# Kernel optimization log

Measured on AMD Instinct MI355X. Metric: run time of the kernel, lower is better.

## Reference

```python
import jax, jax.numpy as jnp
import numpy as np

N_NODES = 50000
N_EDGES = 800000
NFEAT, NHID, NCLASS = 256, 64, 2


def _deg_norm(idx, n_nodes, dtype):
    deg = jax.ops.segment_sum(jnp.ones(idx.shape[0], dtype=dtype), idx, num_segments=n_nodes)
    return jax.lax.rsqrt(jnp.maximum(deg, 1.0))


def gcn_layer(x, W, b, src, dst, n_nodes):
    # DGL GraphConv, norm='both': h = D_in^{-1/2} * Agg( D_out^{-1/2} * x ) W + b
    # weight applied before aggregation (in_feats >= out_feats path); math-equivalent.
    norm_src = _deg_norm(src, n_nodes, x.dtype)  # out-degree norm of source nodes
    norm_dst = _deg_norm(dst, n_nodes, x.dtype)  # in-degree norm of dest nodes
    h = (x * norm_src[:, None]) @ W              # [N, out]
    agg = jax.ops.segment_sum(h[src], dst, num_segments=n_nodes)  # gather + scatter-add
    return agg * norm_dst[:, None] + b


def setup_inputs() -> dict:
    key = jax.random.key(0)
    k1, k2, k3, k4, k5, k6, k7 = jax.random.split(key, 7)
    x = jax.random.normal(k1, (N_NODES, NFEAT), dtype=jnp.float32)
    src = jax.random.randint(k2, (N_EDGES,), 0, N_NODES, dtype=jnp.int64)
    dst = jax.random.randint(k3, (N_EDGES,), 0, N_NODES, dtype=jnp.int64)
    # Glorot-style init like DGL GraphConv
    W1 = jax.random.normal(k4, (NFEAT, NHID), dtype=jnp.float32) * (2.0 / (NFEAT + NHID)) ** 0.5
    b1 = jnp.zeros((NHID,), dtype=jnp.float32)
    W2 = jax.random.normal(k5, (NHID, NCLASS), dtype=jnp.float32) * (2.0 / (NHID + NCLASS)) ** 0.5
    b2 = jnp.zeros((NCLASS,), dtype=jnp.float32)
    return {"x": x, "src": src, "dst": dst, "W1": W1, "b1": b1, "W2": W2, "b2": b2}


def reference(x, src, dst, W1, b1, W2, b2):
    h = jax.nn.relu(gcn_layer(x, W1, b1, src, dst, N_NODES))
    # dropout=False -> p=0, no-op
    logits = gcn_layer(h, W2, b2, src, dst, N_NODES)
    return jax.nn.log_softmax(logits, axis=1)
```

## Files before the change

kernel.cpp:

```cpp
#include <hip/hip_runtime.h>
#include <math.h>

#define N_NODES 50000
#define N_EDGES 800000
#define NFEAT 256
#define NHID 64
#define NCLASS 2

#define DB 64
#define NDB 782
#define BCAP 1536
#define EPB 2048
#define NB_EDGE ((N_EDGES + EPB - 1) / EPB)

#define OFF_CURD 0
#define OFF_CURS 800
#define OFF_RBD  1600
#define OFF_NDST 101600
#define OFF_NSRC 151600
#define OFF_W1T  201600
#define OFF_DPK  209792
#define OFF_SV6  1410944
#define OFF_CSR  1711232
#define OFF_HB   2912384
#define OFF_H2   4512384

typedef __attribute__((ext_vector_type(8))) short bf16x8;
typedef __attribute__((ext_vector_type(8))) short short8;
typedef __attribute__((ext_vector_type(4))) float f32x4;

static __device__ __forceinline__ unsigned short f2bf(float f) {
    union { float f; unsigned int u; } v; v.f = f;
    return (unsigned short)((v.u + 0x8000u) >> 16);
}
static __device__ __forceinline__ unsigned int pk2bf(float f0, float f1) {
    union { float f; unsigned int u; } a, b; a.f = f0; b.f = f1;
    return __builtin_amdgcn_perm(b.u + 0x8000u, a.u + 0x8000u, 0x07060302u);
}
static __device__ __forceinline__ float bflo(unsigned int u) {
    union { unsigned int x; float f; } v; v.x = u << 16; return v.f;
}
static __device__ __forceinline__ float bfhi(unsigned int u) {
    union { unsigned int x; float f; } v; v.x = u & 0xffff0000u; return v.f;
}

#define INIT_N (1600 + NFEAT * NHID)
__global__ __launch_bounds__(256) void init_kernel(const float* __restrict__ W1,
                                                   int* __restrict__ cursors,
                                                   unsigned short* __restrict__ w1t) {
    int g = blockIdx.x * 256 + threadIdx.x;
    if (g < 1600) {
        cursors[g] = 0;
    } else if (g < INIT_N) {
        int idx = g - 1600;
        int k = idx >> 6, n = idx & 63;
        w1t[n * NFEAT + k] = f2bf(W1[idx]);
    }
}

union SgShared {
    struct { int hd[NDB], bd[NDB], cd[NDB], hs[NDB], bs[NDB], cs[NDB]; } b;
    struct { unsigned short As[64][136]; unsigned short Bs[64][136]; } g;
};
__global__ __launch_bounds__(256) void sg_kernel(const int* __restrict__ src,
                                                 const int* __restrict__ dst,
                                                 const float* __restrict__ x,
                                                 const unsigned short* __restrict__ w1t,
                                                 int* __restrict__ cur_d,
                                                 int* __restrict__ cur_s,
                                                 int* __restrict__ dpk,
                                                 unsigned char* __restrict__ sv6,
                                                 unsigned short* __restrict__ hb) {
    __shared__ SgShared su;
    int t = threadIdx.x;
    if (blockIdx.x < NB_EDGE) {
        for (int i = t; i < NDB; i += 256) { su.b.hd[i] = 0; su.b.cd[i] = 0; su.b.hs[i] = 0; su.b.cs[i] = 0; }
        __syncthreads();
        int base = blockIdx.x * EPB;
        int ls[8], ld[8];
#pragma unroll
        for (int i = 0; i < 8; ++i) {
            int e = base + t + i * 256;
            ls[i] = (e < N_EDGES) ? src[e] : -1;
            ld[i] = (e < N_EDGES) ? dst[e] : -1;
            if (ld[i] >= 0) {
                atomicAdd(&su.b.hd[ld[i] >> 6], 1);
                atomicAdd(&su.b.hs[ls[i] >> 6], 1);
            }
        }
        __syncthreads();
        for (int i = t; i < NDB; i += 256) {
            if (su.b.hd[i]) su.b.bd[i] = atomicAdd(&cur_d[i], su.b.hd[i]);
            if (su.b.hs[i]) su.b.bs[i] = atomicAdd(&cur_s[i], su.b.hs[i]);
        }
        __syncthreads();
#pragma unroll
        for (int i = 0; i < 8; ++i) {
            if (ld[i] >= 0) {
                int bin = ld[i] >> 6;
                int pos = su.b.bd[bin] + atomicAdd(&su.b.cd[bin], 1);
                dpk[bin * BCAP + pos] = (ls[i] << 6) | (ld[i] & 63);
                int sbin = ls[i] >> 6;
                int spos = su.b.bs[sbin] + atomicAdd(&su.b.cs[sbin], 1);
                sv6[sbin * BCAP + spos] = (unsigned char)(ls[i] & 63);
            }
        }
    } else {
        const int b = blockIdx.x - NB_EDGE;
        const int row0 = b * 64;
        const int w = t >> 6;
        const int l = t & 63;
        const int m = l & 15;
        const int kq = (l >> 4) * 8;
        const int q = l >> 4;
        f32x4 acc[4] = {{0.f, 0.f, 0.f, 0.f}, {0.f, 0.f, 0.f, 0.f},
                        {0.f, 0.f, 0.f, 0.f}, {0.f, 0.f, 0.f, 0.f}};
#pragma unroll
        for (int half = 0; half < 2; ++half) {
            __syncthreads();
#pragma unroll
            for (int i = 0; i < 8; ++i) {
                int f = i * 256 + t;
                int r = f >> 5;
                int c4 = (f & 31) * 4;
                int grow = row0 + r;
                float4 av = make_float4(0.f, 0.f, 0.f, 0.f);
                if (grow < N_NODES)
                    av = *(const float4*)(&x[(size_t)grow * NFEAT + half * 128 + c4]);
                uint2 o;
                o.x = pk2bf(av.x, av.y);
                o.y = pk2bf(av.z, av.w);
                *(uint2*)(&su.g.As[r][c4]) = o;
            }
#pragma unroll
            for (int i = 0; i < 4; ++i) {
                int c = i * 256 + t;
                int n = c >> 4;
                int k8 = (c & 15) * 8;
                *(short8*)(&su.g.Bs[n][k8]) = *(const short8*)(&w1t[n * NFEAT + half * 128 + k8]);
            }
            __syncthreads();
#pragma unroll
            for (int c8 = 0; c8 < 4; ++c8) {
                int k0 = c8 * 32 + kq;
                bf16x8 a = *(const bf16x8*)(&su.g.As[w * 16 + m][k0]);
#pragma unroll
                for (int ct = 0; ct < 4; ++ct) {
                    bf16x8 bb = *(const bf16x8*)(&su.g.Bs[ct * 16 + m][k0]);
                    acc[ct] = __builtin_amdgcn_mfma_f32_16x16x32_bf16(a, bb, acc[ct], 0, 0, 0);
                }
            }
        }
#pragma unroll
        for (int reg = 0; reg < 4; ++reg) {
            int r = row0 + w * 16 + q * 4 + reg;
            if (r < N_NODES) {
#pragma unroll
                for (int ct = 0; ct < 4; ++ct)
                    hb[(size_t)r * NHID + ct * 16 + m] = f2bf(acc[ct][reg]);
            }
        }
    }
}

union FinShared {
    struct { int ebuf[BCAP]; int hist4[256]; int hist[64]; int seg[64]; int cur[64]; } d;
    struct { int hist4[256]; } s;
};
__global__ __launch_bounds__(256) void fin_kernel(const int* __restrict__ cur_d,
                                                  const int* __restrict__ cur_s,
                                                  const int* __restrict__ dpk,
                                                  const unsigned char* __restrict__ sv6,
                                                  int2* __restrict__ rbdeg,
                                                  float* __restrict__ norm_dst,
                                                  float* __restrict__ norm_src,
                                                  int* __restrict__ csr) {
    __shared__ FinShared su;
    int t = threadIdx.x;
    int role = blockIdx.x & 1;
    int b = blockIdx.x >> 1;

    if (role == 0) {
        su.s.hist4[t] = 0;
        __syncthreads();
        int cnt = cur_s[b];
        int base = b * BCAP;
        int sub = (t & 3) * 64;
        for (int j = t; j < cnt; j += 256) atomicAdd(&su.s.hist4[sub + sv6[base + j]], 1);
        __syncthreads();
        if (t < 64) {
            int gid = b * 64 + t;
            if (gid < N_NODES) {
                int v = su.s.hist4[t] + su.s.hist4[64 + t] + su.s.hist4[128 + t] + su.s.hist4[192 + t];
                norm_src[gid] = rsqrtf(fmaxf((float)v, 1.0f));
            }
        }
    } else {
        int cnt = cur_d[b];
        int base = b * BCAP;
        if (t < 64) { su.d.hist[t] = 0; su.d.cur[t] = 0; }
        su.d.hist4[t] = 0;
        for (int j = t; j < cnt; j += 256) su.d.ebuf[j] = dpk[base + j];
        __syncthreads();
        int sub = (t & 3) * 64;
        for (int j = t; j < cnt; j += 256) atomicAdd(&su.d.hist4[sub + (su.d.ebuf[j] & 63)], 1);
        __syncthreads();
        if (t < 64) {
            int v = su.d.hist4[t] + su.d.hist4[64 + t] + su.d.hist4[128 + t] + su.d.hist4[192 + t];
            su.d.hist[t] = v;
            su.d.seg[t] = v;
        }
        __syncthreads();
#pragma unroll
        for (int off = 1; off < 64; off <<= 1) {
            int xv = 0;
            if (t < 64 && t >= off) xv = su.d.seg[t - off];
            __syncthreads();
            if (t < 64) su.d.seg[t] += xv;
            __syncthreads();
        }
        if (t < 64) {
            int v = su.d.hist[t];
            int excl = su.d.seg[t] - v;
            int gid = b * 64 + t;
            if (gid < N_NODES) {
                rbdeg[gid] = make_int2(base + excl, v);
                norm_dst[gid] = rsqrtf(fmaxf((float)v, 1.0f));
            }
            su.d.seg[t] = excl;
        }
        __syncthreads();
        for (int j = t; j < cnt; j += 256) {
            int p = su.d.ebuf[j];
            int dlow = p & 63;
            int pos = base + su.d.seg[dlow] + atomicAdd(&su.d.cur[dlow], 1);
            csr[pos] = ((unsigned)p) >> 6;
        }
    }
}

__global__ __launch_bounds__(256) void fused1_kernel(const int2* __restrict__ rbdeg,
                                                     const int* __restrict__ csr,
                                                     const unsigned short* __restrict__ hb,
                                                     const float* __restrict__ norm_dst,
                                                     const float* __restrict__ norm_src,
                                                     const float* __restrict__ b1,
                                                     const float* __restrict__ W2,
                                                     float* __restrict__ h2) {
    int gtid = blockIdx.x * blockDim.x + threadIdx.x;
    int node = gtid >> 6;
    int lane = gtid & 63;
    if (node >= N_NODES) return;
    int e8 = lane >> 3, fg = lane & 7;
    int2 rd = rbdeg[node];
    int beg = rd.x;
    int end = beg + rd.y;
    float a0 = 0.f, a1 = 0.f, a2 = 0.f, a3 = 0.f, a4 = 0.f, a5 = 0.f, a6 = 0.f, a7 = 0.f;
    for (int j = beg; j < end; j += 32) {
        int j0 = j + e8, j1 = j0 + 8, j2 = j0 + 16, j3 = j0 + 24;
        uint4 u0 = make_uint4(0u, 0u, 0u, 0u), u1 = make_uint4(0u, 0u, 0u, 0u);
        uint4 u2 = make_uint4(0u, 0u, 0u, 0u), u3 = make_uint4(0u, 0u, 0u, 0u);
        float ns0 = 0.f, ns1 = 0.f, ns2 = 0.f, ns3 = 0.f;
        if (j0 < end) {
            int s = csr[j0];
            ns0 = norm_src[s];
            u0 = *(const uint4*)(&hb[(size_t)s * NHID + fg * 8]);
        }
        if (j1 < end) {
            int s = csr[j1];
            ns1 = norm_src[s];
            u1 = *(const uint4*)(&hb[(size_t)s * NHID + fg * 8]);
        }
        if (j2 < end) {
            int s = csr[j2];
            ns2 = norm_src[s];
            u2 = *(const uint4*)(&hb[(size_t)s * NHID + fg * 8]);
        }
        if (j3 < end) {
            int s = csr[j3];
            ns3 = norm_src[s];
            u3 = *(const uint4*)(&hb[(size_t)s * NHID + fg * 8]);
        }
        a0 = fmaf(ns0, bflo(u0.x), fmaf(ns1, bflo(u1.x), fmaf(ns2, bflo(u2.x), fmaf(ns3, bflo(u3.x), a0))));
        a1 = fmaf(ns0, bfhi(u0.x), fmaf(ns1, bfhi(u1.x), fmaf(ns2, bfhi(u2.x), fmaf(ns3, bfhi(u3.x), a1))));
        a2 = fmaf(ns0, bflo(u0.y), fmaf(ns1, bflo(u1.y), fmaf(ns2, bflo(u2.y), fmaf(ns3, bflo(u3.y), a2))));
        a3 = fmaf(ns0, bfhi(u0.y), fmaf(ns1, bfhi(u1.y), fmaf(ns2, bfhi(u2.y), fmaf(ns3, bfhi(u3.y), a3))));
        a4 = fmaf(ns0, bflo(u0.z), fmaf(ns1, bflo(u1.z), fmaf(ns2, bflo(u2.z), fmaf(ns3, bflo(u3.z), a4))));
        a5 = fmaf(ns0, bfhi(u0.z), fmaf(ns1, bfhi(u1.z), fmaf(ns2, bfhi(u2.z), fmaf(ns3, bfhi(u3.z), a5))));
        a6 = fmaf(ns0, bflo(u0.w), fmaf(ns1, bflo(u1.w), fmaf(ns2, bflo(u2.w), fmaf(ns3, bflo(u3.w), a6))));
        a7 = fmaf(ns0, bfhi(u0.w), fmaf(ns1, bfhi(u1.w), fmaf(ns2, bfhi(u2.w), fmaf(ns3, bfhi(u3.w), a7))));
    }
#pragma unroll
    for (int off = 8; off <= 32; off <<= 1) {
        a0 += __shfl_xor(a0, off, 64);
        a1 += __shfl_xor(a1, off, 64);
        a2 += __shfl_xor(a2, off, 64);
        a3 += __shfl_xor(a3, off, 64);
        a4 += __shfl_xor(a4, off, 64);
        a5 += __shfl_xor(a5, off, 64);
        a6 += __shfl_xor(a6, off, 64);
        a7 += __shfl_xor(a7, off, 64);
    }
    float nd = norm_dst[node], ns = norm_src[node];
    float4 bv0 = *(const float4*)(&b1[fg * 8]);
    float4 bv1 = *(const float4*)(&b1[fg * 8 + 4]);
    float4 w0 = *(const float4*)(&W2[fg * 16 + 0]);
    float4 w1 = *(const float4*)(&W2[fg * 16 + 4]);
    float4 w2v = *(const float4*)(&W2[fg * 16 + 8]);
    float4 w3 = *(const float4*)(&W2[fg * 16 + 12]);
    float h0 = fmaxf(fmaf(a0, nd, bv0.x), 0.f) * ns;
    float h1 = fmaxf(fmaf(a1, nd, bv0.y), 0.f) * ns;
    float h2f = fmaxf(fmaf(a2, nd, bv0.z), 0.f) * ns;
    float h3 = fmaxf(fmaf(a3, nd, bv0.w), 0.f) * ns;
    float h4 = fmaxf(fmaf(a4, nd, bv1.x), 0.f) * ns;
    float h5 = fmaxf(fmaf(a5, nd, bv1.y), 0.f) * ns;
    float h6 = fmaxf(fmaf(a6, nd, bv1.z), 0.f) * ns;
    float h7 = fmaxf(fmaf(a7, nd, bv1.w), 0.f) * ns;
    float p0 = h0 * w0.x + h1 * w0.z + h2f * w1.x + h3 * w1.z +
               h4 * w2v.x + h5 * w2v.z + h6 * w3.x + h7 * w3.z;
    float p1 = h0 * w0.y + h1 * w0.w + h2f * w1.y + h3 * w1.w +
               h4 * w2v.y + h5 * w2v.w + h6 * w3.y + h7 * w3.w;
#pragma unroll
    for (int off = 1; off <= 4; off <<= 1) {
        p0 += __shfl_xor(p0, off, 64);
        p1 += __shfl_xor(p1, off, 64);
    }
    if (lane == 0) *(float2*)(&h2[node * 2]) = make_float2(p0, p1);
}

__global__ __launch_bounds__(256) void fused2_kernel(const int2* __restrict__ rbdeg,
                                                     const int* __restrict__ csr,
                                                     const float* __restrict__ h2,
                                                     const float* __restrict__ norm_dst,
                                                     const float* __restrict__ b2,
                                                     float* __restrict__ out) {
    int gtid = blockIdx.x * blockDim.x + threadIdx.x;
    int n = gtid >> 4;
    int l16 = gtid & 15;
    if (n >= N_NODES) return;
    int2 rd = rbdeg[n];
    int beg = rd.x, end = rd.x + rd.y;
    float s0 = 0.f, s1 = 0.f;
    for (int j = beg + l16; j < end; j += 16) {
        float2 v = *(const float2*)(&h2[csr[j] * 2]);
        s0 += v.x;
        s1 += v.y;
    }
#pragma unroll
    for (int off = 1; off <= 8; off <<= 1) {
        s0 += __shfl_xor(s0, off, 16);
        s1 += __shfl_xor(s1, off, 16);
    }
    if (l16 == 0) {
        float nd = norm_dst[n];
        float l0 = fmaf(s0, nd, b2[0]);
        float l1 = fmaf(s1, nd, b2[1]);
        float m = fmaxf(l0, l1);
        float lse = m + logf(expf(l0 - m) + expf(l1 - m));
        *(float2*)(&out[n * 2]) = make_float2(l0 - lse, l1 - lse);
    }
}

extern "C" void kernel_launch(void* const* d_in, const int* in_sizes, int n_in,
                              void* d_out, int out_size, void* d_ws, size_t ws_size,
                              hipStream_t stream) {
    const float* x  = (const float*)d_in[0];
    const int* src  = (const int*)d_in[1];
    const int* dst  = (const int*)d_in[2];
    const float* W1 = (const float*)d_in[3];
    const float* b1 = (const float*)d_in[4];
    const float* W2 = (const float*)d_in[5];
    const float* b2 = (const float*)d_in[6];
    float* out = (float*)d_out;
    float* ws  = (float*)d_ws;
    int*   wsi = (int*)d_ws;

    int*   cur_d    = wsi + OFF_CURD;
    int*   cur_s    = wsi + OFF_CURS;
    int2*  rbdeg    = (int2*)(wsi + OFF_RBD);
    float* norm_dst = ws + OFF_NDST;
    float* norm_src = ws + OFF_NSRC;
    unsigned short* w1t = (unsigned short*)(wsi + OFF_W1T);
    int*   dpk      = wsi + OFF_DPK;
    unsigned char* sv6 = (unsigned char*)(wsi + OFF_SV6);
    int*   csr      = wsi + OFF_CSR;
    unsigned short* hb = (unsigned short*)(wsi + OFF_HB);
    float* h2       = ws + OFF_H2;

    init_kernel<<<(INIT_N + 255) / 256, 256, 0, stream>>>(W1, cur_d, w1t);
    sg_kernel<<<NB_EDGE + NDB, 256, 0, stream>>>(src, dst, x, w1t, cur_d, cur_s, dpk, sv6, hb);
    fin_kernel<<<NDB * 2, 256, 0, stream>>>(cur_d, cur_s, dpk, sv6, rbdeg, norm_dst, norm_src, csr);
    {
        long long threads = (long long)N_NODES * 64;
        fused1_kernel<<<(int)((threads + 255) / 256), 256, 0, stream>>>(
            rbdeg, csr, hb, norm_dst, norm_src, b1, W2, h2);
    }
    {
        long long threads = (long long)N_NODES * 16;
        fused2_kernel<<<(int)((threads + 255) / 256), 256, 0, stream>>>(
            rbdeg, csr, h2, norm_dst, b2, out);
    }
}
```

Baseline: 165.8 us.

## Count source degrees with global atomics, interleave edge and GEMM blocks

Source out-degrees are now counted with per-node global atomics. This replaces binning source low bits into a byte buffer followed by a separate histogram pass, so the source-binning writes and half of the finalize blocks go away. The first-layer GEMM blocks drop LDS staging and read x and the transposed W1 straight from global memory into MFMA operands. Edge-binning blocks are interleaved one-in-three with GEMM blocks, and dst cursors are padded to separate cache lines. The trade-off is random global atomic contention on 50k counters and uncoalesced per-lane GEMM loads, which may miss the reuse that LDS staging gave.

```diff
diff --git a/kernel.cpp b/kernel.cpp
--- a/kernel.cpp
+++ b/kernel.cpp
@@ -12,18 +12,18 @@
 #define BCAP 1536
 #define EPB 2048
 #define NB_EDGE ((N_EDGES + EPB - 1) / EPB)
+#define CSTRIDE 32
 
 #define OFF_CURD 0
-#define OFF_CURS 800
-#define OFF_RBD  1600
-#define OFF_NDST 101600
-#define OFF_NSRC 151600
-#define OFF_W1T  201600
-#define OFF_DPK  209792
-#define OFF_SV6  1410944
-#define OFF_CSR  1711232
-#define OFF_HB   2912384
-#define OFF_H2   4512384
+#define OFF_DEGS 25024
+#define OFF_RBD  75024
+#define OFF_NDST 175024
+#define OFF_NSRC 225024
+#define OFF_W1T  275024
+#define OFF_DPK  283216
+#define OFF_CSR  1484368
+#define OFF_HB   2685520
+#define OFF_H2   4285520
 
 typedef __attribute__((ext_vector_type(8))) short bf16x8;
 typedef __attribute__((ext_vector_type(8))) short short8;
@@ -44,39 +44,41 @@
     union { unsigned int x; float f; } v; v.x = u & 0xffff0000u; return v.f;
 }
 
-#define INIT_N (1600 + NFEAT * NHID)
+#define INIT_CUR (NDB * CSTRIDE)
+#define INIT_N (INIT_CUR + N_NODES + NFEAT * NHID)
 __global__ __launch_bounds__(256) void init_kernel(const float* __restrict__ W1,
-                                                   int* __restrict__ cursors,
+                                                   int* __restrict__ cur_d,
+                                                   int* __restrict__ deg_src,
                                                    unsigned short* __restrict__ w1t) {
     int g = blockIdx.x * 256 + threadIdx.x;
-    if (g < 1600) {
-        cursors[g] = 0;
+    if (g < INIT_CUR) {
+        cur_d[g] = 0;
+    } else if (g < INIT_CUR + N_NODES) {
+        deg_src[g - INIT_CUR] = 0;
     } else if (g < INIT_N) {
-        int idx = g - 1600;
+        int idx = g - INIT_CUR - N_NODES;
         int k = idx >> 6, n = idx & 63;
         w1t[n * NFEAT + k] = f2bf(W1[idx]);
     }
 }
 
-union SgShared {
-    struct { int hd[NDB], bd[NDB], cd[NDB], hs[NDB], bs[NDB], cs[NDB]; } b;
-    struct { unsigned short As[64][136]; unsigned short Bs[64][136]; } g;
-};
+struct SgShared { int hd[NDB], bd[NDB], cd[NDB]; };
 __global__ __launch_bounds__(256) void sg_kernel(const int* __restrict__ src,
                                                  const int* __restrict__ dst,
                                                  const float* __restrict__ x,
                                                  const unsigned short* __restrict__ w1t,
                                                  int* __restrict__ cur_d,
-                                                 int* __restrict__ cur_s,
+                                                 int* __restrict__ deg_src,
                                                  int* __restrict__ dpk,
-                                                 unsigned char* __restrict__ sv6,
                                                  unsigned short* __restrict__ hb) {
     __shared__ SgShared su;
     int t = threadIdx.x;
-    if (blockIdx.x < NB_EDGE) {
-        for (int i = t; i < NDB; i += 256) { su.b.hd[i] = 0; su.b.cd[i] = 0; su.b.hs[i] = 0; su.b.cs[i] = 0; }
-        __syncthreads();
-        int base = blockIdx.x * EPB;
+    int bid = blockIdx.x;
+    if (bid % 3 == 0) {
+        int eb = bid / 3;
+        for (int i = t; i < NDB; i += 256) { su.hd[i] = 0; su.cd[i] = 0; }
+        __syncthreads();
+        int base = eb * EPB;
         int ls[8], ld[8];
 #pragma unroll
         for (int i = 0; i < 8; ++i) {
@@ -84,71 +86,47 @@
             ls[i] = (e < N_EDGES) ? src[e] : -1;
             ld[i] = (e < N_EDGES) ? dst[e] : -1;
             if (ld[i] >= 0) {
-                atomicAdd(&su.b.hd[ld[i] >> 6], 1);
-                atomicAdd(&su.b.hs[ls[i] >> 6], 1);
+                atomicAdd(&su.hd[ld[i] >> 6], 1);
+                atomicAdd(&deg_src[ls[i]], 1);
             }
         }
         __syncthreads();
-        for (int i = t; i < NDB; i += 256) {
-            if (su.b.hd[i]) su.b.bd[i] = atomicAdd(&cur_d[i], su.b.hd[i]);
-            if (su.b.hs[i]) su.b.bs[i] = atomicAdd(&cur_s[i], su.b.hs[i]);
-        }
+        for (int i = t; i < NDB; i += 256)
+            if (su.hd[i]) su.bd[i] = atomicAdd(&cur_d[i * CSTRIDE], su.hd[i]);
         __syncthreads();
 #pragma unroll
         for (int i = 0; i < 8; ++i) {
             if (ld[i] >= 0) {
                 int bin = ld[i] >> 6;
-                int pos = su.b.bd[bin] + atomicAdd(&su.b.cd[bin], 1);
+                int pos = su.bd[bin] + atomicAdd(&su.cd[bin], 1);
                 dpk[bin * BCAP + pos] = (ls[i] << 6) | (ld[i] & 63);
-                int sbin = ls[i] >> 6;
-                int spos = su.b.bs[sbin] + atomicAdd(&su.b.cs[sbin], 1);
-                sv6[sbin * BCAP + spos] = (unsigned char)(ls[i] & 63);
             }
         }
     } else {
-        const int b = blockIdx.x - NB_EDGE;
+        const int b = (bid / 3) * 2 + (bid % 3) - 1;
         const int row0 = b * 64;
         const int w = t >> 6;
         const int l = t & 63;
         const int m = l & 15;
-        const int kq = (l >> 4) * 8;
         const int q = l >> 4;
+        int grow = row0 + w * 16 + m;
+        const float* xr = &x[(size_t)((grow < N_NODES) ? grow : 0) * NFEAT];
         f32x4 acc[4] = {{0.f, 0.f, 0.f, 0.f}, {0.f, 0.f, 0.f, 0.f},
                         {0.f, 0.f, 0.f, 0.f}, {0.f, 0.f, 0.f, 0.f}};
 #pragma unroll
-        for (int half = 0; half < 2; ++half) {
-            __syncthreads();
-#pragma unroll
-            for (int i = 0; i < 8; ++i) {
-                int f = i * 256 + t;
-                int r = f >> 5;
-                int c4 = (f & 31) * 4;
-                int grow = row0 + r;
-                float4 av = make_float4(0.f, 0.f, 0.f, 0.f);
-                if (grow < N_NODES)
-                    av = *(const float4*)(&x[(size_t)grow * NFEAT + half * 128 + c4]);
-                uint2 o;
-                o.x = pk2bf(av.x, av.y);
-                o.y = pk2bf(av.z, av.w);
-                *(uint2*)(&su.g.As[r][c4]) = o;
-            }
-#pragma unroll
-            for (int i = 0; i < 4; ++i) {
-                int c = i * 256 + t;
-                int n = c >> 4;
-                int k8 = (c & 15) * 8;
-                *(short8*)(&su.g.Bs[n][k8]) = *(const short8*)(&w1t[n * NFEAT + half * 128 + k8]);
-            }
-            __syncthreads();
-#pragma unroll
-            for (int c8 = 0; c8 < 4; ++c8) {
-                int k0 = c8 * 32 + kq;
-                bf16x8 a = *(const bf16x8*)(&su.g.As[w * 16 + m][k0]);
-#pragma unroll
-                for (int ct = 0; ct < 4; ++ct) {
-                    bf16x8 bb = *(const bf16x8*)(&su.g.Bs[ct * 16 + m][k0]);
-                    acc[ct] = __builtin_amdgcn_mfma_f32_16x16x32_bf16(a, bb, acc[ct], 0, 0, 0);
-                }
+        for (int c8 = 0; c8 < 8; ++c8) {
+            int k0 = c8 * 32 + q * 8;
+            float4 av0 = *(const float4*)(xr + k0);
+            float4 av1 = *(const float4*)(xr + k0 + 4);
+            union { bf16x8 v; unsigned int u[4]; } a;
+            a.u[0] = pk2bf(av0.x, av0.y);
+            a.u[1] = pk2bf(av0.z, av0.w);
+            a.u[2] = pk2bf(av1.x, av1.y);
+            a.u[3] = pk2bf(av1.z, av1.w);
+#pragma unroll
+            for (int ct = 0; ct < 4; ++ct) {
+                bf16x8 bb = *(const bf16x8*)(&w1t[(ct * 16 + m) * NFEAT + k0]);
+                acc[ct] = __builtin_amdgcn_mfma_f32_16x16x32_bf16(a.v, bb, acc[ct], 0, 0, 0);
             }
         }
 #pragma unroll
@@ -163,79 +141,57 @@
     }
 }
 
-union FinShared {
-    struct { int ebuf[BCAP]; int hist4[256]; int hist[64]; int seg[64]; int cur[64]; } d;
-    struct { int hist4[256]; } s;
-};
+struct FinShared { int ebuf[BCAP]; int hist4[256]; int hist[64]; int seg[64]; int cur[64]; };
 __global__ __launch_bounds__(256) void fin_kernel(const int* __restrict__ cur_d,
-                                                  const int* __restrict__ cur_s,
+                                                  const int* __restrict__ deg_src,
                                                   const int* __restrict__ dpk,
-                                                  const unsigned char* __restrict__ sv6,
                                                   int2* __restrict__ rbdeg,
                                                   float* __restrict__ norm_dst,
                                                   float* __restrict__ norm_src,
                                                   int* __restrict__ csr) {
     __shared__ FinShared su;
     int t = threadIdx.x;
-    int role = blockIdx.x & 1;
-    int b = blockIdx.x >> 1;
-
-    if (role == 0) {
-        su.s.hist4[t] = 0;
-        __syncthreads();
-        int cnt = cur_s[b];
-        int base = b * BCAP;
-        int sub = (t & 3) * 64;
-        for (int j = t; j < cnt; j += 256) atomicAdd(&su.s.hist4[sub + sv6[base + j]], 1);
-        __syncthreads();
-        if (t < 64) {
-            int gid = b * 64 + t;
-            if (gid < N_NODES) {
-                int v = su.s.hist4[t] + su.s.hist4[64 + t] + su.s.hist4[128 + t] + su.s.hist4[192 + t];
-                norm_src[gid] = rsqrtf(fmaxf((float)v, 1.0f));
-            }
-        }
-    } else {
-        int cnt = cur_d[b];
-        int base = b * BCAP;
-        if (t < 64) { su.d.hist[t] = 0; su.d.cur[t] = 0; }
-        su.d.hist4[t] = 0;
-        for (int j = t; j < cnt; j += 256) su.d.ebuf[j] = dpk[base + j];
-        __syncthreads();
-        int sub = (t & 3) * 64;
-        for (int j = t; j < cnt; j += 256) atomicAdd(&su.d.hist4[sub + (su.d.ebuf[j] & 63)], 1);
-        __syncthreads();
-        if (t < 64) {
-            int v = su.d.hist4[t] + su.d.hist4[64 + t] + su.d.hist4[128 + t] + su.d.hist4[192 + t];
-            su.d.hist[t] = v;
-            su.d.seg[t] = v;
-        }
-        __syncthreads();
-#pragma unroll
-        for (int off = 1; off < 64; off <<= 1) {
-            int xv = 0;
-            if (t < 64 && t >= off) xv = su.d.seg[t - off];
-            __syncthreads();
-            if (t < 64) su.d.seg[t] += xv;
-            __syncthreads();
-        }
-        if (t < 64) {
-            int v = su.d.hist[t];
-            int excl = su.d.seg[t] - v;
-            int gid = b * 64 + t;
-            if (gid < N_NODES) {
-                rbdeg[gid] = make_int2(base + excl, v);
-                norm_dst[gid] = rsqrtf(fmaxf((float)v, 1.0f));
-            }
-            su.d.seg[t] = excl;
-        }
-        __syncthreads();
-        for (int j = t; j < cnt; j += 256) {
-            int p = su.d.ebuf[j];
-            int dlow = p & 63;
-            int pos = base + su.d.seg[dlow] + atomicAdd(&su.d.cur[dlow], 1);
-            csr[pos] = ((unsigned)p) >> 6;
-        }
+    int b = blockIdx.x;
+    int cnt = cur_d[b * CSTRIDE];
+    int base = b * BCAP;
+    if (t < 64) { su.hist[t] = 0; su.cur[t] = 0; }
+    su.hist4[t] = 0;
+    for (int j = t; j < cnt; j += 256) su.ebuf[j] = dpk[base + j];
+    __syncthreads();
+    int sub = (t & 3) * 64;
+    for (int j = t; j < cnt; j += 256) atomicAdd(&su.hist4[sub + (su.ebuf[j] & 63)], 1);
+    __syncthreads();
+    if (t < 64) {
+        int v = su.hist4[t] + su.hist4[64 + t] + su.hist4[128 + t] + su.hist4[192 + t];
+        su.hist[t] = v;
+        su.seg[t] = v;
+    }
+    __syncthreads();
+#pragma unroll
+    for (int off = 1; off < 64; off <<= 1) {
+        int xv = 0;
+        if (t < 64 && t >= off) xv = su.seg[t - off];
+        __syncthreads();
+        if (t < 64) su.seg[t] += xv;
+        __syncthreads();
+    }
+    if (t < 64) {
+        int v = su.hist[t];
+        int excl = su.seg[t] - v;
+        int gid = b * 64 + t;
+        if (gid < N_NODES) {
+            rbdeg[gid] = make_int2(base + excl, v);
+            norm_dst[gid] = rsqrtf(fmaxf((float)v, 1.0f));
+            norm_src[gid] = rsqrtf(fmaxf((float)deg_src[gid], 1.0f));
+        }
+        su.seg[t] = excl;
+    }
+    __syncthreads();
+    for (int j = t; j < cnt; j += 256) {
+        int p = su.ebuf[j];
+        int dlow = p & 63;
+        int pos = base + su.seg[dlow] + atomicAdd(&su.cur[dlow], 1);
+        csr[pos] = ((unsigned)p) >> 6;
     }
 }
 
@@ -376,20 +332,19 @@
     int*   wsi = (int*)d_ws;
 
     int*   cur_d    = wsi + OFF_CURD;
-    int*   cur_s    = wsi + OFF_CURS;
+    int*   deg_src  = wsi + OFF_DEGS;
     int2*  rbdeg    = (int2*)(wsi + OFF_RBD);
     float* norm_dst = ws + OFF_NDST;
     float* norm_src = ws + OFF_NSRC;
     unsigned short* w1t = (unsigned short*)(wsi + OFF_W1T);
     int*   dpk      = wsi + OFF_DPK;
-    unsigned char* sv6 = (unsigned char*)(wsi + OFF_SV6);
     int*   csr      = wsi + OFF_CSR;
     unsigned short* hb = (unsigned short*)(wsi + OFF_HB);
     float* h2       = ws + OFF_H2;
 
-    init_kernel<<<(INIT_N + 255) / 256, 256, 0, stream>>>(W1, cur_d, w1t);
-    sg_kernel<<<NB_EDGE + NDB, 256, 0, stream>>>(src, dst, x, w1t, cur_d, cur_s, dpk, sv6, hb);
-    fin_kernel<<<NDB * 2, 256, 0, stream>>>(cur_d, cur_s, dpk, sv6, rbdeg, norm_dst, norm_src, csr);
+    init_kernel<<<(INIT_N + 255) / 256, 256, 0, stream>>>(W1, cur_d, deg_src, w1t);
+    sg_kernel<<<NB_EDGE + NDB, 256, 0, stream>>>(src, dst, x, w1t, cur_d, deg_src, dpk, hb);
+    fin_kernel<<<NDB, 256, 0, stream>>>(cur_d, deg_src, dpk, rbdeg, norm_dst, norm_src, csr);
     {
         long long threads = (long long)N_NODES * 64;
         fused1_kernel<<<(int)((threads + 255) / 256), 256, 0, stream>>>(
```

Result: slower. 190.8 us (+15.1%).

## Interleave edge-binning and GEMM blocks, pad atomic cursors, drop LDS staging in GEMM

Applied to the files above, without the earlier changes.

Edge-binning blocks and node-GEMM blocks are now interleaved in a 1:2 pattern across the grid, so the scatter-heavy and compute-heavy work share the GPU instead of running in sequence. Global bin cursors are spaced 32 ints apart to cut same-cache-line atomic contention. The GEMM path now loads x rows and the transposed W1 straight from global memory into MFMA operands, with no LDS tiles and no barriers; this shrinks shared memory but relies on cache for reuse of W1. The CSR buffer is aliased onto the dpk region to shrink the workspace, which is only safe if each bin's CSR writes stay inside data already read into shared memory.

```diff
diff --git a/kernel.cpp b/kernel.cpp
--- a/kernel.cpp
+++ b/kernel.cpp
@@ -12,18 +12,18 @@
 #define BCAP 1536
 #define EPB 2048
 #define NB_EDGE ((N_EDGES + EPB - 1) / EPB)
+#define CSTRIDE 32
 
 #define OFF_CURD 0
-#define OFF_CURS 800
-#define OFF_RBD  1600
-#define OFF_NDST 101600
-#define OFF_NSRC 151600
-#define OFF_W1T  201600
-#define OFF_DPK  209792
-#define OFF_SV6  1410944
-#define OFF_CSR  1711232
-#define OFF_HB   2912384
-#define OFF_H2   4512384
+#define OFF_CURS 25024
+#define OFF_RBD  50048
+#define OFF_NDST 150048
+#define OFF_NSRC 200048
+#define OFF_W1T  250048
+#define OFF_DPK  258240
+#define OFF_SV6  1459392
+#define OFF_HB   1759680
+#define OFF_H2   3359680
 
 typedef __attribute__((ext_vector_type(8))) short bf16x8;
 typedef __attribute__((ext_vector_type(8))) short short8;
@@ -44,24 +44,22 @@
     union { unsigned int x; float f; } v; v.x = u & 0xffff0000u; return v.f;
 }
 
-#define INIT_N (1600 + NFEAT * NHID)
+#define INIT_CUR (2 * NDB * CSTRIDE)
+#define INIT_N (INIT_CUR + NFEAT * NHID)
 __global__ __launch_bounds__(256) void init_kernel(const float* __restrict__ W1,
                                                    int* __restrict__ cursors,
                                                    unsigned short* __restrict__ w1t) {
     int g = blockIdx.x * 256 + threadIdx.x;
-    if (g < 1600) {
+    if (g < INIT_CUR) {
         cursors[g] = 0;
     } else if (g < INIT_N) {
-        int idx = g - 1600;
+        int idx = g - INIT_CUR;
         int k = idx >> 6, n = idx & 63;
         w1t[n * NFEAT + k] = f2bf(W1[idx]);
     }
 }
 
-union SgShared {
-    struct { int hd[NDB], bd[NDB], cd[NDB], hs[NDB], bs[NDB], cs[NDB]; } b;
-    struct { unsigned short As[64][136]; unsigned short Bs[64][136]; } g;
-};
+struct SgShared { int hd[NDB], bd[NDB], cd[NDB], hs[NDB], bs[NDB], cs[NDB]; };
 __global__ __launch_bounds__(256) void sg_kernel(const int* __restrict__ src,
                                                  const int* __restrict__ dst,
                                                  const float* __restrict__ x,
@@ -73,10 +71,12 @@
                                                  unsigned short* __restrict__ hb) {
     __shared__ SgShared su;
     int t = threadIdx.x;
-    if (blockIdx.x < NB_EDGE) {
-        for (int i = t; i < NDB; i += 256) { su.b.hd[i] = 0; su.b.cd[i] = 0; su.b.hs[i] = 0; su.b.cs[i] = 0; }
-        __syncthreads();
-        int base = blockIdx.x * EPB;
+    int bid = blockIdx.x;
+    if (bid % 3 == 0) {
+        int eb = bid / 3;
+        for (int i = t; i < NDB; i += 256) { su.hd[i] = 0; su.cd[i] = 0; su.hs[i] = 0; su.cs[i] = 0; }
+        __syncthreads();
+        int base = eb * EPB;
         int ls[8], ld[8];
 #pragma unroll
         for (int i = 0; i < 8; ++i) {
@@ -84,71 +84,52 @@
             ls[i] = (e < N_EDGES) ? src[e] : -1;
             ld[i] = (e < N_EDGES) ? dst[e] : -1;
             if (ld[i] >= 0) {
-                atomicAdd(&su.b.hd[ld[i] >> 6], 1);
-                atomicAdd(&su.b.hs[ls[i] >> 6], 1);
+                atomicAdd(&su.hd[ld[i] >> 6], 1);
+                atomicAdd(&su.hs[ls[i] >> 6], 1);
             }
         }
         __syncthreads();
         for (int i = t; i < NDB; i += 256) {
-            if (su.b.hd[i]) su.b.bd[i] = atomicAdd(&cur_d[i], su.b.hd[i]);
-            if (su.b.hs[i]) su.b.bs[i] = atomicAdd(&cur_s[i], su.b.hs[i]);
+            if (su.hd[i]) su.bd[i] = atomicAdd(&cur_d[i * CSTRIDE], su.hd[i]);
+            if (su.hs[i]) su.bs[i] = atomicAdd(&cur_s[i * CSTRIDE], su.hs[i]);
         }
         __syncthreads();
 #pragma unroll
         for (int i = 0; i < 8; ++i) {
             if (ld[i] >= 0) {
                 int bin = ld[i] >> 6;
-                int pos = su.b.bd[bin] + atomicAdd(&su.b.cd[bin], 1);
+                int pos = su.bd[bin] + atomicAdd(&su.cd[bin], 1);
                 dpk[bin * BCAP + pos] = (ls[i] << 6) | (ld[i] & 63);
                 int sbin = ls[i] >> 6;
-                int spos = su.b.bs[sbin] + atomicAdd(&su.b.cs[sbin], 1);
+                int spos = su.bs[sbin] + atomicAdd(&su.cs[sbin], 1);
                 sv6[sbin * BCAP + spos] = (unsigned char)(ls[i] & 63);
             }
         }
     } else {
-        const int b = blockIdx.x - NB_EDGE;
+        const int b = (bid / 3) * 2 + (bid % 3) - 1;
         const int row0 = b * 64;
         const int w = t >> 6;
         const int l = t & 63;
         const int m = l & 15;
-        const int kq = (l >> 4) * 8;
         const int q = l >> 4;
+        int grow = row0 + w * 16 + m;
+        const float* xr = &x[(size_t)((grow < N_NODES) ? grow : 0) * NFEAT];
         f32x4 acc[4] = {{0.f, 0.f, 0.f, 0.f}, {0.f, 0.f, 0.f, 0.f},
                         {0.f, 0.f, 0.f, 0.f}, {0.f, 0.f, 0.f, 0.f}};
 #pragma unroll
-        for (int half = 0; half < 2; ++half) {
-            __syncthreads();
-#pragma unroll
-            for (int i = 0; i < 8; ++i) {
-                int f = i * 256 + t;
-                int r = f >> 5;
-                int c4 = (f & 31) * 4;
-                int grow = row0 + r;
-                float4 av = make_float4(0.f, 0.f, 0.f, 0.f);
-                if (grow < N_NODES)
-                    av = *(const float4*)(&x[(size_t)grow * NFEAT + half * 128 + c4]);
-                uint2 o;
-                o.x = pk2bf(av.x, av.y);
-                o.y = pk2bf(av.z, av.w);
-                *(uint2*)(&su.g.As[r][c4]) = o;
-            }
-#pragma unroll
-            for (int i = 0; i < 4; ++i) {
-                int c = i * 256 + t;
-                int n = c >> 4;
-                int k8 = (c & 15) * 8;
-                *(short8*)(&su.g.Bs[n][k8]) = *(const short8*)(&w1t[n * NFEAT + half * 128 + k8]);
-            }
-            __syncthreads();
-#pragma unroll
-            for (int c8 = 0; c8 < 4; ++c8) {
-                int k0 = c8 * 32 + kq;
-                bf16x8 a = *(const bf16x8*)(&su.g.As[w * 16 + m][k0]);
-#pragma unroll
-                for (int ct = 0; ct < 4; ++ct) {
-                    bf16x8 bb = *(const bf16x8*)(&su.g.Bs[ct * 16 + m][k0]);
-                    acc[ct] = __builtin_amdgcn_mfma_f32_16x16x32_bf16(a, bb, acc[ct], 0, 0, 0);
-                }
+        for (int c8 = 0; c8 < 8; ++c8) {
+            int k0 = c8 * 32 + q * 8;
+            float4 av0 = *(const float4*)(xr + k0);
+            float4 av1 = *(const float4*)(xr + k0 + 4);
+            union { bf16x8 v; unsigned int u[4]; } a;
+            a.u[0] = pk2bf(av0.x, av0.y);
+            a.u[1] = pk2bf(av0.z, av0.w);
+            a.u[2] = pk2bf(av1.x, av1.y);
+            a.u[3] = pk2bf(av1.z, av1.w);
+#pragma unroll
+            for (int ct = 0; ct < 4; ++ct) {
+                bf16x8 bb = *(const bf16x8*)(&w1t[(ct * 16 + m) * NFEAT + k0]);
+                acc[ct] = __builtin_amdgcn_mfma_f32_16x16x32_bf16(a.v, bb, acc[ct], 0, 0, 0);
             }
         }
 #pragma unroll
@@ -183,7 +164,7 @@
     if (role == 0) {
         su.s.hist4[t] = 0;
         __syncthreads();
-        int cnt = cur_s[b];
+        int cnt = cur_s[b * CSTRIDE];
         int base = b * BCAP;
         int sub = (t & 3) * 64;
         for (int j = t; j < cnt; j += 256) atomicAdd(&su.s.hist4[sub + sv6[base + j]], 1);
@@ -196,7 +177,7 @@
             }
         }
     } else {
-        int cnt = cur_d[b];
+        int cnt = cur_d[b * CSTRIDE];
         int base = b * BCAP;
         if (t < 64) { su.d.hist[t] = 0; su.d.cur[t] = 0; }
         su.d.hist4[t] = 0;
@@ -383,12 +364,12 @@
     unsigned short* w1t = (unsigned short*)(wsi + OFF_W1T);
     int*   dpk      = wsi + OFF_DPK;
     unsigned char* sv6 = (unsigned char*)(wsi + OFF_SV6);
-    int*   csr      = wsi + OFF_CSR;
+    int*   csr      = wsi + OFF_DPK;
     unsigned short* hb = (unsigned short*)(wsi + OFF_HB);
     float* h2       = ws + OFF_H2;
 
     init_kernel<<<(INIT_N + 255) / 256, 256, 0, stream>>>(W1, cur_d, w1t);
-    sg_kernel<<<NB_EDGE + NDB, 256, 0, stream>>>(src, dst, x, w1t, cur_d, cur_s, dpk, sv6, hb);
+    sg_kernel<<<NB_EDGE * 3, 256, 0, stream>>>(src, dst, x, w1t, cur_d, cur_s, dpk, sv6, hb);
     fin_kernel<<<NDB * 2, 256, 0, stream>>>(cur_d, cur_s, dpk, sv6, rbdeg, norm_dst, norm_src, csr);
     {
         long long threads = (long long)N_NODES * 64;
```

After: 178.4 us. 7.6% more time.
